# Kernel tuning notes

Measured on AMD Instinct MI355X. Metric: run time of the kernel, lower is better.

The kernel has to match this reference:

```python
import jax, jax.numpy as jnp
import numpy as np

EPS = 1.55e-5  # tf.math.l2_normalize epsilon semantics: x / sqrt(max(sum(x^2), eps))


def _l2norm_tokens(t):
    # normalize over the token axis (-2), matching tf.math.l2_normalize(axis=-2)
    sq = jnp.sum(t * t, axis=-2, keepdims=True)
    return t * jax.lax.rsqrt(jnp.maximum(sq, EPS))


def setup_inputs() -> dict:
    key = jax.random.key(0)
    ks = jax.random.split(key, 4)
    B, H, W, C = 16, 64, 64, 512
    heads = 8
    return {
        "x": jax.random.normal(ks[0], (B, H, W, C), jnp.float32),
        "qkv_w": jax.random.normal(ks[1], (C, 3 * C), jnp.float32) * (C ** -0.5),
        "q_bias": jnp.zeros((C,), jnp.float32),
        "v_bias": jnp.zeros((C,), jnp.float32),
        "scale": jnp.ones((heads, 1, 1), jnp.float32),
        "proj_w": jax.random.normal(ks[2], (C, C), jnp.float32) * (C ** -0.5),
        "proj_b": jnp.zeros((C,), jnp.float32),
    }


def reference(x, qkv_w, q_bias, v_bias, scale, proj_w, proj_b):
    B, H, W, C = x.shape
    heads = scale.shape[0]
    d = C // heads
    N = H * W

    # 1x1 conv QKV (no conv bias) + concatenated [q_bias, 0, v_bias]
    qkv = jnp.einsum("bhwc,cf->bhwf", x, qkv_w)
    qkv = qkv + jnp.concatenate([q_bias, jnp.zeros_like(q_bias), v_bias])
    # [B, N, heads, 3, d] -> [B, heads, N, 3, d]
    qkv = qkv.reshape(B, N, heads, 3, d).transpose(0, 2, 1, 3, 4)
    q, k, v = qkv[..., 0, :], qkv[..., 1, :], qkv[..., 2, :]  # each [B, heads, N, d]

    q = _l2norm_tokens(q)
    k = _l2norm_tokens(k)

    # channel-attention: [B, heads, d, d]
    attn = jnp.einsum("bhnd,bhne->bhde", q * jnp.exp(scale), k)
    attn = jax.nn.softmax(attn, axis=-1)

    # matmul(attn, v^T) -> [B, heads, d, N]; perm [0,3,1,2] -> [B, N, heads, d]
    out = jnp.einsum("bhde,bhne->bhdn", attn, v)
    out = out.transpose(0, 3, 1, 2).reshape(B, H, W, C)

    # output 1x1 conv projection with bias
    return jnp.einsum("bhwc,cf->bhwf", out, proj_w) + proj_b
```

## Files before the change

kernel.cpp:

```cpp
#include <hip/hip_runtime.h>
#include <stdint.h>
#include <stddef.h>

#define BATCH  16
#define HEADS  8
#define NTOK   4096
#define CDIM   512
#define FDIM   1536

typedef short bf16x8 __attribute__((ext_vector_type(8)));
typedef float fx4    __attribute__((ext_vector_type(4)));

__device__ __forceinline__ uint16_t f2bf(float f) {
    uint32_t u = __float_as_uint(f);
    return (uint16_t)((u + 0x7FFFu + ((u >> 16) & 1u)) >> 16);
}
__device__ __forceinline__ float bf2f(uint16_t u) {
    return __uint_as_float(((uint32_t)u) << 16);
}
__device__ __forceinline__ void gload16(const uint16_t* g, uint16_t* l) {
    __builtin_amdgcn_global_load_lds(
        (const __attribute__((address_space(1))) uint32_t*)(g),
        (__attribute__((address_space(3))) uint32_t*)(l), 16, 0, 0);
}
__device__ __forceinline__ int cidx(int row, int col) {
    return row * 128 + (col ^ ((row & 7) << 3));
}

__global__ void transpose_w_kernel(const float* __restrict__ qkv_w,
                                   const float* __restrict__ proj_w,
                                   uint16_t* __restrict__ Wt,
                                   uint16_t* __restrict__ Pt) {
    __shared__ uint16_t tile[32][33];
    int blk = blockIdx.x;
    const float* src; uint16_t* dst; int W, Hh, r0, c0;
    if (blk < 768) {
        int tr = blk / 48, tc = blk % 48;
        src = qkv_w; dst = Wt; W = 1536; Hh = 512; r0 = tr * 32; c0 = tc * 32;
    } else {
        blk -= 768;
        int tr = blk / 16, tc = blk % 16;
        src = proj_w; dst = Pt; W = 512; Hh = 512; r0 = tr * 32; c0 = tc * 32;
    }
    const int tx = threadIdx.x & 31, ty = threadIdx.x >> 5;
    #pragma unroll
    for (int j = 0; j < 4; j++)
        tile[ty + 8 * j][tx] = f2bf(src[(size_t)(r0 + ty + 8 * j) * W + c0 + tx]);
    __syncthreads();
    #pragma unroll
    for (int j = 0; j < 4; j++)
        dst[(size_t)(c0 + ty + 8 * j) * Hh + r0 + tx] = tile[tx][ty + 8 * j];
}

__global__ void prep_kernel(const float* __restrict__ X,
                            uint16_t* __restrict__ Xb,
                            float* __restrict__ Sqk) {
    const int tid = blockIdx.x * blockDim.x + threadIdx.x;
    const int stride = gridDim.x * blockDim.x;
    for (int i = tid; i < (1 << 22); i += stride) {
        const fx4* src = reinterpret_cast<const fx4*>(X + (size_t)i * 8);
        fx4 v0 = src[0], v1 = src[1];
        union { bf16x8 v; uint16_t u[8]; } pk;
        #pragma unroll
        for (int e = 0; e < 4; e++) { pk.u[e] = f2bf(v0[e]); pk.u[4 + e] = f2bf(v1[e]); }
        reinterpret_cast<bf16x8*>(Xb)[i] = pk.v;
    }
    for (int i = tid; i < 16384; i += stride) Sqk[i] = 0.0f;
}

__global__ __launch_bounds__(256) void gemm_qkv_kernel(
        const uint16_t* __restrict__ Xb, const uint16_t* __restrict__ Wt,
        const float* __restrict__ q_bias, const float* __restrict__ v_bias,
        uint16_t* __restrict__ QT, uint16_t* __restrict__ KT,
        uint16_t* __restrict__ VT,
        float* __restrict__ Sq, float* __restrict__ Sk) {
    __shared__ uint16_t ring[4][8192];
    const int bx = blockIdx.x;
    const int swz = (bx & 7) * 768 + (bx >> 3);
    const int tm = swz / 12, tn = swz % 12;
    const int gm = tm * 128, gn = tn * 128;
    const int b = gm >> 12, tok0 = gm & 4095;
    const int t = threadIdx.x, lane = t & 63, w = t >> 6;
    const int wm = w >> 1, wn = w & 1;
    const int l15 = lane & 15, lg = lane >> 4;
    fx4 acc[4][4] = {};
    const int srow = t >> 2;
    const int scol = (((t & 3) ^ (srow & 3)) << 3);
    const uint16_t* gA = Xb + (size_t)(gm + srow) * 512 + scol;
    const uint16_t* gB = Wt + (size_t)(gn + srow) * 512 + scol;
#define STAGE_QKV(kt_) do {                                                   \
        const int s_ = (kt_) & 3; const int k0_ = (kt_) * 32;                 \
        gload16(gA + k0_,                 &ring[s_][t * 8]);                  \
        gload16(gA + (size_t)64*512 + k0_, &ring[s_][t * 8 + 2048]);          \
        gload16(gB + k0_,                 &ring[s_][4096 + t * 8]);           \
        gload16(gB + (size_t)64*512 + k0_, &ring[s_][4096 + t * 8 + 2048]);   \
    } while (0)
    STAGE_QKV(0); STAGE_QKV(1); STAGE_QKV(2);
    #pragma unroll
    for (int kt = 0; kt < 16; ++kt) {
        if (kt < 14)       asm volatile("s_waitcnt vmcnt(8) lgkmcnt(0)" ::: "memory");
        else if (kt == 14) asm volatile("s_waitcnt vmcnt(4) lgkmcnt(0)" ::: "memory");
        else               asm volatile("s_waitcnt vmcnt(0) lgkmcnt(0)" ::: "memory");
        __builtin_amdgcn_s_barrier();
        if (kt < 13) STAGE_QKV(kt + 3);
        const uint16_t* As = &ring[kt & 3][0];
        const uint16_t* Bs = &ring[kt & 3][4096];
        bf16x8 af[4], bfr[4];
        #pragma unroll
        for (int m = 0; m < 4; m++) {
            const int row = wm * 64 + m * 16 + l15;
            af[m] = *reinterpret_cast<const bf16x8*>(&As[row * 32 + ((lg ^ (row & 3)) << 3)]);
        }
        #pragma unroll
        for (int n = 0; n < 4; n++) {
            const int row = wn * 64 + n * 16 + l15;
            bfr[n] = *reinterpret_cast<const bf16x8*>(&Bs[row * 32 + ((lg ^ (row & 3)) << 3)]);
        }
        __builtin_amdgcn_s_setprio(1);
        #pragma unroll
        for (int m = 0; m < 4; m++)
            #pragma unroll
            for (int n = 0; n < 4; n++)
                acc[m][n] = __builtin_amdgcn_mfma_f32_16x16x32_bf16(
                    af[m], bfr[n], acc[m][n], 0, 0, 0);
        __builtin_amdgcn_s_setprio(0);
    }
#undef STAGE_QKV
    __syncthreads();
    uint16_t* sh = &ring[0][0];
    #pragma unroll
    for (int n = 0; n < 4; n++) {
        const int col = gn + wn * 64 + n * 16 + l15;
        const float bias = (col < 512) ? q_bias[col]
                          : ((col < 1024) ? 0.0f : v_bias[col - 1024]);
        #pragma unroll
        for (int m = 0; m < 4; m++)
            #pragma unroll
            for (int r = 0; r < 4; r++) {
                const int lrow = wm * 64 + m * 16 + lg * 4 + r;
                const int lcol = wn * 64 + n * 16 + l15;
                sh[cidx(lrow, lcol)] = f2bf(acc[m][n][r] + bias);
            }
    }
    __syncthreads();
    const int cc = t >> 7, tloc = t & 127;
    const int u = (gn >> 6) + cc;
    const int h = u / 3, which = u % 3;
    const int bh = b * 8 + h;
    if (which < 2) {
        const int d = tloc & 63, oct = tloc >> 6;
        uint16_t* dst = (which == 0 ? QT : KT)
                        + ((size_t)bh * 64 + d) * 4096 + tok0 + oct * 64;
        float ss = 0.f;
        #pragma unroll
        for (int g = 0; g < 8; g++) {
            union { bf16x8 v; uint16_t u16v[8]; } pk;
            #pragma unroll
            for (int s2 = 0; s2 < 8; s2++) {
                uint16_t val = sh[cidx(oct * 64 + g * 8 + s2, cc * 64 + d)];
                pk.u16v[s2] = val;
                float f = bf2f(val);
                ss += f * f;
            }
            *reinterpret_cast<bf16x8*>(dst + g * 8) = pk.v;
        }
        atomicAdd((which == 0 ? Sq : Sk) + bh * 64 + d, ss);
    } else {
        const int tok = tloc;
        uint16_t* dst = VT + (size_t)(gm + tok) * 512 + h * 64;
        #pragma unroll
        for (int bb = 0; bb < 8; bb++) {
            bf16x8 v = *reinterpret_cast<const bf16x8*>(&sh[cidx(tok, cc * 64 + bb * 8)]);
            *reinterpret_cast<bf16x8*>(dst + bb * 8) = v;
        }
    }
}

__global__ __launch_bounds__(256) void attn_qk_kernel(
        const uint16_t* __restrict__ QT, const uint16_t* __restrict__ KT,
        float* __restrict__ Gpart) {
    __shared__ uint16_t Qs[64 * 128];
    __shared__ uint16_t Ks[64 * 128];
    const int blk = blockIdx.x;
    const int bh = blk >> 2, quarter = blk & 3;
    const int t = threadIdx.x, lane = t & 63, w = t >> 6;
    const int l15 = lane & 15, lg = lane >> 4;
    const int wr = w >> 1, wc = w & 1;
    fx4 acc[2][2] = {};
    const uint16_t* qbase = QT + (size_t)bh * 64 * 4096;
    const uint16_t* kbase = KT + (size_t)bh * 64 * 4096;
    for (int it = 0; it < 8; it++) {
        const int tokt = quarter * 1024 + it * 128;
        #pragma unroll
        for (int j = 0; j < 4; j++) {
            const int li = j * 256 + t;
            const int row = li >> 4;
            const int src_off = (((li & 15) ^ (row & 7)) << 3);
            gload16(qbase + (size_t)row * 4096 + tokt + src_off, &Qs[li * 8]);
            gload16(kbase + (size_t)row * 4096 + tokt + src_off, &Ks[li * 8]);
        }
        __syncthreads();
        #pragma unroll
        for (int ks = 0; ks < 4; ks++) {
            const int kof = ks * 32 + lg * 8;
            const int ra0 = wr * 32 + l15,      ra1 = wr * 32 + 16 + l15;
            const int rb0 = wc * 32 + l15,      rb1 = wc * 32 + 16 + l15;
            bf16x8 a0 = *reinterpret_cast<const bf16x8*>(&Qs[ra0 * 128 + (kof ^ ((ra0 & 7) << 3))]);
            bf16x8 a1 = *reinterpret_cast<const bf16x8*>(&Qs[ra1 * 128 + (kof ^ ((ra1 & 7) << 3))]);
            bf16x8 b0 = *reinterpret_cast<const bf16x8*>(&Ks[rb0 * 128 + (kof ^ ((rb0 & 7) << 3))]);
            bf16x8 b1 = *reinterpret_cast<const bf16x8*>(&Ks[rb1 * 128 + (kof ^ ((rb1 & 7) << 3))]);
            acc[0][0] = __builtin_amdgcn_mfma_f32_16x16x32_bf16(a0, b0, acc[0][0], 0, 0, 0);
            acc[0][1] = __builtin_amdgcn_mfma_f32_16x16x32_bf16(a0, b1, acc[0][1], 0, 0, 0);
            acc[1][0] = __builtin_amdgcn_mfma_f32_16x16x32_bf16(a1, b0, acc[1][0], 0, 0, 0);
            acc[1][1] = __builtin_amdgcn_mfma_f32_16x16x32_bf16(a1, b1, acc[1][1], 0, 0, 0);
        }
        __syncthreads();
    }
    float* gp = Gpart + (size_t)quarter * 524288 + (size_t)bh * 4096;
    #pragma unroll
    for (int mi = 0; mi < 2; mi++)
        #pragma unroll
        for (int ni = 0; ni < 2; ni++)
            #pragma unroll
            for (int r = 0; r < 4; r++) {
                const int d = wr * 32 + mi * 16 + lg * 4 + r;
                const int e = wc * 32 + ni * 16 + l15;
                gp[d * 64 + e] = acc[mi][ni][r];
            }
}

__global__ void attn_finalize_kernel(const float* __restrict__ Gpart,
                                     const float* __restrict__ Sq,
                                     const float* __restrict__ Sk,
                                     const float* __restrict__ scale,
                                     uint16_t* __restrict__ attnb) {
    const int bh = blockIdx.x;
    const int h = bh & 7;
    const int t = threadIdx.x;
    const int e = t & 63, w = t >> 6;
    const float es = expf(scale[h]);
    const float rk = rsqrtf(fmaxf(Sk[bh * 64 + e], 1.55e-5f));
    const float* g0 = Gpart + (size_t)bh * 4096;
    for (int d = w; d < 64; d += 4) {
        const float rq = rsqrtf(fmaxf(Sq[bh * 64 + d], 1.55e-5f));
        float g = g0[d * 64 + e] + g0[524288 + d * 64 + e]
                + g0[1048576 + d * 64 + e] + g0[1572864 + d * 64 + e];
        float x = es * g * rq * rk;
        float m = x;
        #pragma unroll
        for (int off = 32; off; off >>= 1) m = fmaxf(m, __shfl_xor(m, off, 64));
        float p = expf(x - m);
        float s = p;
        #pragma unroll
        for (int off = 32; off; off >>= 1) s += __shfl_xor(s, off, 64);
        attnb[(size_t)bh * 4096 + d * 64 + e] = f2bf(p / s);
    }
}

__global__ __launch_bounds__(256) void pv_kernel(
        const uint16_t* __restrict__ VT, const uint16_t* __restrict__ attnb,
        uint16_t* __restrict__ out_t) {
    __shared__ uint16_t Vs[64 * 64];
    __shared__ uint16_t Os[64 * 64];
    const int blk = blockIdx.x;
    const int bh = blk >> 6, chunk = blk & 63;
    const int b = bh >> 3, h = bh & 7;
    const int n0 = chunk * 64;
    const int t = threadIdx.x, lane = t & 63, w = t >> 6;
    const int l15 = lane & 15, lg = lane >> 4;
    #pragma unroll
    for (int j = 0; j < 2; j++) {
        const int li = j * 256 + t;
        const int row = li >> 3;
        const int src_off = (((li & 7) ^ (row & 7)) << 3);
        gload16(VT + (size_t)(b * NTOK + n0 + row) * 512 + h * 64 + src_off, &Vs[li * 8]);
    }
    bf16x8 bfr[4][2];
    const uint16_t* ab = attnb + (size_t)bh * 4096;
    #pragma unroll
    for (int n = 0; n < 4; n++)
        #pragma unroll
        for (int ks = 0; ks < 2; ks++)
            bfr[n][ks] = *reinterpret_cast<const bf16x8*>(ab + (n * 16 + l15) * 64 + ks * 32 + lg * 8);
    __syncthreads();
    fx4 acc[4] = {};
    #pragma unroll
    for (int ks = 0; ks < 2; ks++) {
        const int row = w * 16 + l15;
        const int kof = ks * 32 + lg * 8;
        bf16x8 a = *reinterpret_cast<const bf16x8*>(&Vs[row * 64 + (kof ^ ((row & 7) << 3))]);
        #pragma unroll
        for (int n = 0; n < 4; n++)
            acc[n] = __builtin_amdgcn_mfma_f32_16x16x32_bf16(a, bfr[n][ks], acc[n], 0, 0, 0);
    }
    #pragma unroll
    for (int n = 0; n < 4; n++)
        #pragma unroll
        for (int r = 0; r < 4; r++) {
            const int row = w * 16 + lg * 4 + r;
            const int col = n * 16 + l15;
            Os[row * 64 + (col ^ ((row & 7) << 3))] = f2bf(acc[n][r]);
        }
    __syncthreads();
    {
        const int tr = t >> 2, c0 = (t & 3) * 16;
        uint16_t* orow = out_t + (size_t)(b * NTOK + n0 + tr) * CDIM + h * 64;
        #pragma unroll
        for (int cc2 = 0; cc2 < 2; cc2++) {
            const int c = c0 + cc2 * 8;
            const int chnk = (c >> 3) ^ (tr & 7);
            bf16x8 vv = *reinterpret_cast<const bf16x8*>(&Os[tr * 64 + (chnk << 3)]);
            *reinterpret_cast<bf16x8*>(orow + c) = vv;
        }
    }
}

__global__ __launch_bounds__(256) void gemm_proj_kernel(
        const uint16_t* __restrict__ At, const uint16_t* __restrict__ Pt,
        const float* __restrict__ proj_b, float* __restrict__ outp) {
    __shared__ uint16_t ring[4][8192];
    const int bx = blockIdx.x;
    const int swz = (bx & 7) * 256 + (bx >> 3);
    const int tn = swz & 3, tm = swz >> 2;
    const int gm = tm * 128, gn = tn * 128;
    const int t = threadIdx.x, lane = t & 63, w = t >> 6;
    const int wm = w >> 1, wn = w & 1;
    const int l15 = lane & 15, lg = lane >> 4;
    fx4 acc[4][4] = {};
    const int srow = t >> 2;
    const int scol = (((t & 3) ^ (srow & 3)) << 3);
    const uint16_t* gA = At + (size_t)(gm + srow) * 512 + scol;
    const uint16_t* gB = Pt + (size_t)(gn + srow) * 512 + scol;
#define STAGE_PROJ(kt_) do {                                                  \
        const int s_ = (kt_) & 3; const int k0_ = (kt_) * 32;                 \
        gload16(gA + k0_,                 &ring[s_][t * 8]);                  \
        gload16(gA + (size_t)64*512 + k0_, &ring[s_][t * 8 + 2048]);          \
        gload16(gB + k0_,                 &ring[s_][4096 + t * 8]);           \
        gload16(gB + (size_t)64*512 + k0_, &ring[s_][4096 + t * 8 + 2048]);   \
    } while (0)
    STAGE_PROJ(0); STAGE_PROJ(1); STAGE_PROJ(2);
    #pragma unroll
    for (int kt = 0; kt < 16; ++kt) {
        if (kt < 14)       asm volatile("s_waitcnt vmcnt(8) lgkmcnt(0)" ::: "memory");
        else if (kt == 14) asm volatile("s_waitcnt vmcnt(4) lgkmcnt(0)" ::: "memory");
        else               asm volatile("s_waitcnt vmcnt(0) lgkmcnt(0)" ::: "memory");
        __builtin_amdgcn_s_barrier();
        if (kt < 13) STAGE_PROJ(kt + 3);
        const uint16_t* As = &ring[kt & 3][0];
        const uint16_t* Bs = &ring[kt & 3][4096];
        bf16x8 af[4], bfr[4];
        #pragma unroll
        for (int m = 0; m < 4; m++) {
            const int row = wm * 64 + m * 16 + l15;
            af[m] = *reinterpret_cast<const bf16x8*>(&As[row * 32 + ((lg ^ (row & 3)) << 3)]);
        }
        #pragma unroll
        for (int n = 0; n < 4; n++) {
            const int row = wn * 64 + n * 16 + l15;
            bfr[n] = *reinterpret_cast<const bf16x8*>(&Bs[row * 32 + ((lg ^ (row & 3)) << 3)]);
        }
        __builtin_amdgcn_s_setprio(1);
        #pragma unroll
        for (int m = 0; m < 4; m++)
            #pragma unroll
            for (int n = 0; n < 4; n++)
                acc[m][n] = __builtin_amdgcn_mfma_f32_16x16x32_bf16(
                    af[m], bfr[n], acc[m][n], 0, 0, 0);
        __builtin_amdgcn_s_setprio(0);
    }
#undef STAGE_PROJ
    #pragma unroll
    for (int m = 0; m < 4; m++) {
        #pragma unroll
        for (int n = 0; n < 4; n++) {
            const int col = gn + wn * 64 + n * 16 + l15;
            const float bias = proj_b[col];
            #pragma unroll
            for (int r = 0; r < 4; r++) {
                const int row = gm + wm * 64 + m * 16 + lg * 4 + r;
                outp[(size_t)row * CDIM + col] = acc[m][n][r] + bias;
            }
        }
    }
}

extern "C" void kernel_launch(void* const* d_in, const int* in_sizes, int n_in,
                              void* d_out, int out_size, void* d_ws, size_t ws_size,
                              hipStream_t stream) {
    (void)in_sizes; (void)n_in; (void)out_size; (void)ws_size;
    const float* x      = (const float*)d_in[0];
    const float* qkv_w  = (const float*)d_in[1];
    const float* q_bias = (const float*)d_in[2];
    const float* v_bias = (const float*)d_in[3];
    const float* scale  = (const float*)d_in[4];
    const float* proj_w = (const float*)d_in[5];
    const float* proj_b = (const float*)d_in[6];
    float* out = (float*)d_out;

    char* wsp = (char*)d_ws;
    uint16_t* Wt    = (uint16_t*)(wsp);
    uint16_t* Pt    = (uint16_t*)(wsp + 1572864);
    float*    Sq    = (float*)   (wsp + 2097152);
    float*    Sk    = (float*)   (wsp + 2129920);
    float*    Gpart = (float*)   (wsp + 2162688);
    uint16_t* attnb = (uint16_t*)(wsp + 10551296);
    uint16_t* QT    = (uint16_t*)(wsp + 11599872);
    uint16_t* KT    = (uint16_t*)(wsp + 78708736);
    uint16_t* VT    = (uint16_t*)(wsp + 145817600);
    uint16_t* Xb    = (uint16_t*)(wsp + 212926464);
    uint16_t* out_t = Xb;

    hipLaunchKernelGGL(transpose_w_kernel, dim3(1024), dim3(256), 0, stream,
                       qkv_w, proj_w, Wt, Pt);
    hipLaunchKernelGGL(prep_kernel, dim3(2048), dim3(256), 0, stream,
                       x, Xb, Sq);
    hipLaunchKernelGGL(gemm_qkv_kernel, dim3(6144), dim3(256), 0, stream,
                       Xb, Wt, q_bias, v_bias, QT, KT, VT, Sq, Sk);
    hipLaunchKernelGGL(attn_qk_kernel, dim3(512), dim3(256), 0, stream,
                       QT, KT, Gpart);
    hipLaunchKernelGGL(attn_finalize_kernel, dim3(128), dim3(256), 0, stream,
                       Gpart, Sq, Sk, scale, attnb);
    hipLaunchKernelGGL(pv_kernel, dim3(8192), dim3(256), 0, stream,
                       VT, attnb, out_t);
    hipLaunchKernelGGL(gemm_proj_kernel, dim3(2048), dim3(256), 0, stream,
                       out_t, Pt, proj_b, out);
}
```

Before: 545.5 us.

## Shrink GEMM rings to three stages, store Q/K directly, double-buffer QK loads

The QKV and projection GEMMs drop from a 4-stage to a 3-stage LDS ring (prefetch distance 2). This cuts shared memory per block from 64KB to 48KB so more blocks can be resident. The QKV epilogue now writes Q/K straight from accumulators with 8-byte stores and a shuffle-reduced sum of squares, staging only V through LDS. It also computes the norm from fp32 values rather than rounded bf16. attn_qk gains a double-buffered LDS pipeline so the next token tile loads while the current one computes, at the cost of doubled LDS there.

```diff
diff --git a/kernel.cpp b/kernel.cpp
--- a/kernel.cpp
+++ b/kernel.cpp
@@ -22,9 +22,6 @@
     __builtin_amdgcn_global_load_lds(
         (const __attribute__((address_space(1))) uint32_t*)(g),
         (__attribute__((address_space(3))) uint32_t*)(l), 16, 0, 0);
-}
-__device__ __forceinline__ int cidx(int row, int col) {
-    return row * 128 + (col ^ ((row & 7) << 3));
 }
 
 __global__ void transpose_w_kernel(const float* __restrict__ qkv_w,
@@ -74,7 +71,7 @@
         uint16_t* __restrict__ QT, uint16_t* __restrict__ KT,
         uint16_t* __restrict__ VT,
         float* __restrict__ Sq, float* __restrict__ Sk) {
-    __shared__ uint16_t ring[4][8192];
+    __shared__ uint16_t ring[3][8192];
     const int bx = blockIdx.x;
     const int swz = (bx & 7) * 768 + (bx >> 3);
     const int tm = swz / 12, tn = swz % 12;
@@ -88,23 +85,23 @@
     const int scol = (((t & 3) ^ (srow & 3)) << 3);
     const uint16_t* gA = Xb + (size_t)(gm + srow) * 512 + scol;
     const uint16_t* gB = Wt + (size_t)(gn + srow) * 512 + scol;
-#define STAGE_QKV(kt_) do {                                                   \
-        const int s_ = (kt_) & 3; const int k0_ = (kt_) * 32;                 \
-        gload16(gA + k0_,                 &ring[s_][t * 8]);                  \
-        gload16(gA + (size_t)64*512 + k0_, &ring[s_][t * 8 + 2048]);          \
-        gload16(gB + k0_,                 &ring[s_][4096 + t * 8]);           \
-        gload16(gB + (size_t)64*512 + k0_, &ring[s_][4096 + t * 8 + 2048]);   \
-    } while (0)
-    STAGE_QKV(0); STAGE_QKV(1); STAGE_QKV(2);
+    auto stage = [&](int kt_) {
+        const int s_ = kt_ % 3;
+        const int k0_ = kt_ * 32;
+        gload16(gA + k0_,                    &ring[s_][t * 8]);
+        gload16(gA + (size_t)64 * 512 + k0_, &ring[s_][t * 8 + 2048]);
+        gload16(gB + k0_,                    &ring[s_][4096 + t * 8]);
+        gload16(gB + (size_t)64 * 512 + k0_, &ring[s_][4096 + t * 8 + 2048]);
+    };
+    stage(0); stage(1);
     #pragma unroll
     for (int kt = 0; kt < 16; ++kt) {
-        if (kt < 14)       asm volatile("s_waitcnt vmcnt(8) lgkmcnt(0)" ::: "memory");
-        else if (kt == 14) asm volatile("s_waitcnt vmcnt(4) lgkmcnt(0)" ::: "memory");
-        else               asm volatile("s_waitcnt vmcnt(0) lgkmcnt(0)" ::: "memory");
+        if (kt < 15) asm volatile("s_waitcnt vmcnt(4) lgkmcnt(0)" ::: "memory");
+        else         asm volatile("s_waitcnt vmcnt(0) lgkmcnt(0)" ::: "memory");
         __builtin_amdgcn_s_barrier();
-        if (kt < 13) STAGE_QKV(kt + 3);
-        const uint16_t* As = &ring[kt & 3][0];
-        const uint16_t* Bs = &ring[kt & 3][4096];
+        if (kt < 14) stage(kt + 2);
+        const uint16_t* As = &ring[kt % 3][0];
+        const uint16_t* Bs = &ring[kt % 3][4096];
         bf16x8 af[4], bfr[4];
         #pragma unroll
         for (int m = 0; m < 4; m++) {
@@ -125,53 +122,72 @@
                     af[m], bfr[n], acc[m][n], 0, 0, 0);
         __builtin_amdgcn_s_setprio(0);
     }
-#undef STAGE_QKV
     __syncthreads();
-    uint16_t* sh = &ring[0][0];
+    const int u = (gn >> 6) + wn;
+    const int type = u % 3;
+    const int h = u / 3;
+    const int bh = b * 8 + h;
+    float biasn[4];
     #pragma unroll
     for (int n = 0; n < 4; n++) {
         const int col = gn + wn * 64 + n * 16 + l15;
-        const float bias = (col < 512) ? q_bias[col]
-                          : ((col < 1024) ? 0.0f : v_bias[col - 1024]);
-        #pragma unroll
-        for (int m = 0; m < 4; m++)
-            #pragma unroll
-            for (int r = 0; r < 4; r++) {
-                const int lrow = wm * 64 + m * 16 + lg * 4 + r;
-                const int lcol = wn * 64 + n * 16 + l15;
-                sh[cidx(lrow, lcol)] = f2bf(acc[m][n][r] + bias);
+        biasn[n] = (col < 512) ? q_bias[col]
+                  : ((col < 1024) ? 0.0f : v_bias[col - 1024]);
+    }
+    if (type < 2) {
+        uint16_t* T = (type == 0) ? QT : KT;
+        #pragma unroll
+        for (int n = 0; n < 4; n++) {
+            const int d = n * 16 + l15;
+            uint16_t* dst = T + ((size_t)bh * 64 + d) * 4096 + tok0 + wm * 64 + lg * 4;
+            float ss = 0.f;
+            #pragma unroll
+            for (int m = 0; m < 4; m++) {
+                union { uint16_t u4[4]; uint64_t q; } pk;
+                #pragma unroll
+                for (int r = 0; r < 4; r++) {
+                    const float f = acc[m][n][r] + biasn[n];
+                    pk.u4[r] = f2bf(f);
+                    ss += f * f;
+                }
+                *reinterpret_cast<uint64_t*>(dst + m * 16) = pk.q;
             }
+            ss += __shfl_xor(ss, 16, 64);
+            ss += __shfl_xor(ss, 32, 64);
+            if (lg == 0)
+                atomicAdd((type == 0 ? Sq : Sk) + bh * 64 + d, ss);
+        }
+    } else {
+        uint16_t* vs = &ring[0][0];
+        #pragma unroll
+        for (int n = 0; n < 4; n++) {
+            const int lcol = n * 16 + l15;
+            #pragma unroll
+            for (int m = 0; m < 4; m++)
+                #pragma unroll
+                for (int r = 0; r < 4; r++) {
+                    const int lrow = wm * 64 + m * 16 + lg * 4 + r;
+                    vs[lrow * 64 + (lcol ^ ((lrow & 7) << 3))] =
+                        f2bf(acc[m][n][r] + biasn[n]);
+                }
+        }
     }
     __syncthreads();
-    const int cc = t >> 7, tloc = t & 127;
-    const int u = (gn >> 6) + cc;
-    const int h = u / 3, which = u % 3;
-    const int bh = b * 8 + h;
-    if (which < 2) {
-        const int d = tloc & 63, oct = tloc >> 6;
-        uint16_t* dst = (which == 0 ? QT : KT)
-                        + ((size_t)bh * 64 + d) * 4096 + tok0 + oct * 64;
-        float ss = 0.f;
-        #pragma unroll
-        for (int g = 0; g < 8; g++) {
-            union { bf16x8 v; uint16_t u16v[8]; } pk;
-            #pragma unroll
-            for (int s2 = 0; s2 < 8; s2++) {
-                uint16_t val = sh[cidx(oct * 64 + g * 8 + s2, cc * 64 + d)];
-                pk.u16v[s2] = val;
-                float f = bf2f(val);
-                ss += f * f;
+    {
+        const int u0 = gn >> 6;
+        const int uv = (u0 % 3 == 2) ? u0 : (((u0 + 1) % 3 == 2) ? (u0 + 1) : -1);
+        if (uv >= 0) {
+            const uint16_t* vs = &ring[0][0];
+            const int hv = uv / 3;
+            const int row = t >> 1, c0v = (t & 1) * 32;
+            uint16_t* dst = VT + (size_t)(gm + row) * 512 + hv * 64 + c0v;
+            #pragma unroll
+            for (int cc = 0; cc < 4; cc++) {
+                const int col = c0v + cc * 8;
+                bf16x8 vv = *reinterpret_cast<const bf16x8*>(
+                    &vs[row * 64 + (col ^ ((row & 7) << 3))]);
+                *reinterpret_cast<bf16x8*>(dst + cc * 8) = vv;
             }
-            *reinterpret_cast<bf16x8*>(dst + g * 8) = pk.v;
-        }
-        atomicAdd((which == 0 ? Sq : Sk) + bh * 64 + d, ss);
-    } else {
-        const int tok = tloc;
-        uint16_t* dst = VT + (size_t)(gm + tok) * 512 + h * 64;
-        #pragma unroll
-        for (int bb = 0; bb < 8; bb++) {
-            bf16x8 v = *reinterpret_cast<const bf16x8*>(&sh[cidx(tok, cc * 64 + bb * 8)]);
-            *reinterpret_cast<bf16x8*>(dst + bb * 8) = v;
         }
     }
 }
@@ -179,8 +195,8 @@
 __global__ __launch_bounds__(256) void attn_qk_kernel(
         const uint16_t* __restrict__ QT, const uint16_t* __restrict__ KT,
         float* __restrict__ Gpart) {
-    __shared__ uint16_t Qs[64 * 128];
-    __shared__ uint16_t Ks[64 * 128];
+    __shared__ uint16_t Qs[2][8192];
+    __shared__ uint16_t Ks[2][8192];
     const int blk = blockIdx.x;
     const int bh = blk >> 2, quarter = blk & 3;
     const int t = threadIdx.x, lane = t & 63, w = t >> 6;
@@ -189,32 +205,40 @@
     fx4 acc[2][2] = {};
     const uint16_t* qbase = QT + (size_t)bh * 64 * 4096;
     const uint16_t* kbase = KT + (size_t)bh * 64 * 4096;
-    for (int it = 0; it < 8; it++) {
-        const int tokt = quarter * 1024 + it * 128;
+    auto stage = [&](int it_) {
+        const int tokt = quarter * 1024 + it_ * 128;
+        uint16_t* qd = &Qs[it_ & 1][0];
+        uint16_t* kd = &Ks[it_ & 1][0];
         #pragma unroll
         for (int j = 0; j < 4; j++) {
             const int li = j * 256 + t;
             const int row = li >> 4;
             const int src_off = (((li & 15) ^ (row & 7)) << 3);
-            gload16(qbase + (size_t)row * 4096 + tokt + src_off, &Qs[li * 8]);
-            gload16(kbase + (size_t)row * 4096 + tokt + src_off, &Ks[li * 8]);
-        }
-        __syncthreads();
+            gload16(qbase + (size_t)row * 4096 + tokt + src_off, qd + li * 8);
+            gload16(kbase + (size_t)row * 4096 + tokt + src_off, kd + li * 8);
+        }
+    };
+    stage(0);
+    for (int it = 0; it < 8; it++) {
+        asm volatile("s_waitcnt vmcnt(0) lgkmcnt(0)" ::: "memory");
+        __builtin_amdgcn_s_barrier();
+        if (it < 7) stage(it + 1);
+        const uint16_t* Qb = &Qs[it & 1][0];
+        const uint16_t* Kb = &Ks[it & 1][0];
         #pragma unroll
         for (int ks = 0; ks < 4; ks++) {
             const int kof = ks * 32 + lg * 8;
             const int ra0 = wr * 32 + l15,      ra1 = wr * 32 + 16 + l15;
             const int rb0 = wc * 32 + l15,      rb1 = wc * 32 + 16 + l15;
-            bf16x8 a0 = *reinterpret_cast<const bf16x8*>(&Qs[ra0 * 128 + (kof ^ ((ra0 & 7) << 3))]);
-            bf16x8 a1 = *reinterpret_cast<const bf16x8*>(&Qs[ra1 * 128 + (kof ^ ((ra1 & 7) << 3))]);
-            bf16x8 b0 = *reinterpret_cast<const bf16x8*>(&Ks[rb0 * 128 + (kof ^ ((rb0 & 7) << 3))]);
-            bf16x8 b1 = *reinterpret_cast<const bf16x8*>(&Ks[rb1 * 128 + (kof ^ ((rb1 & 7) << 3))]);
+            bf16x8 a0 = *reinterpret_cast<const bf16x8*>(&Qb[ra0 * 128 + (kof ^ ((ra0 & 7) << 3))]);
+            bf16x8 a1 = *reinterpret_cast<const bf16x8*>(&Qb[ra1 * 128 + (kof ^ ((ra1 & 7) << 3))]);
+            bf16x8 b0 = *reinterpret_cast<const bf16x8*>(&Kb[rb0 * 128 + (kof ^ ((rb0 & 7) << 3))]);
+            bf16x8 b1 = *reinterpret_cast<const bf16x8*>(&Kb[rb1 * 128 + (kof ^ ((rb1 & 7) << 3))]);
             acc[0][0] = __builtin_amdgcn_mfma_f32_16x16x32_bf16(a0, b0, acc[0][0], 0, 0, 0);
             acc[0][1] = __builtin_amdgcn_mfma_f32_16x16x32_bf16(a0, b1, acc[0][1], 0, 0, 0);
             acc[1][0] = __builtin_amdgcn_mfma_f32_16x16x32_bf16(a1, b0, acc[1][0], 0, 0, 0);
             acc[1][1] = __builtin_amdgcn_mfma_f32_16x16x32_bf16(a1, b1, acc[1][1], 0, 0, 0);
         }
-        __syncthreads();
     }
     float* gp = Gpart + (size_t)quarter * 524288 + (size_t)bh * 4096;
     #pragma unroll
@@ -318,7 +342,7 @@
 __global__ __launch_bounds__(256) void gemm_proj_kernel(
         const uint16_t* __restrict__ At, const uint16_t* __restrict__ Pt,
         const float* __restrict__ proj_b, float* __restrict__ outp) {
-    __shared__ uint16_t ring[4][8192];
+    __shared__ uint16_t ring[3][8192];
     const int bx = blockIdx.x;
     const int swz = (bx & 7) * 256 + (bx >> 3);
     const int tn = swz & 3, tm = swz >> 2;
@@ -331,23 +355,23 @@
     const int scol = (((t & 3) ^ (srow & 3)) << 3);
     const uint16_t* gA = At + (size_t)(gm + srow) * 512 + scol;
     const uint16_t* gB = Pt + (size_t)(gn + srow) * 512 + scol;
-#define STAGE_PROJ(kt_) do {                                                  \
-        const int s_ = (kt_) & 3; const int k0_ = (kt_) * 32;                 \
-        gload16(gA + k0_,                 &ring[s_][t * 8]);                  \
-        gload16(gA + (size_t)64*512 + k0_, &ring[s_][t * 8 + 2048]);          \
-        gload16(gB + k0_,                 &ring[s_][4096 + t * 8]);           \
-        gload16(gB + (size_t)64*512 + k0_, &ring[s_][4096 + t * 8 + 2048]);   \
-    } while (0)
-    STAGE_PROJ(0); STAGE_PROJ(1); STAGE_PROJ(2);
+    auto stage = [&](int kt_) {
+        const int s_ = kt_ % 3;
+        const int k0_ = kt_ * 32;
+        gload16(gA + k0_,                    &ring[s_][t * 8]);
+        gload16(gA + (size_t)64 * 512 + k0_, &ring[s_][t * 8 + 2048]);
+        gload16(gB + k0_,                    &ring[s_][4096 + t * 8]);
+        gload16(gB + (size_t)64 * 512 + k0_, &ring[s_][4096 + t * 8 + 2048]);
+    };
+    stage(0); stage(1);
     #pragma unroll
     for (int kt = 0; kt < 16; ++kt) {
-        if (kt < 14)       asm volatile("s_waitcnt vmcnt(8) lgkmcnt(0)" ::: "memory");
-        else if (kt == 14) asm volatile("s_waitcnt vmcnt(4) lgkmcnt(0)" ::: "memory");
-        else               asm volatile("s_waitcnt vmcnt(0) lgkmcnt(0)" ::: "memory");
+        if (kt < 15) asm volatile("s_waitcnt vmcnt(4) lgkmcnt(0)" ::: "memory");
+        else         asm volatile("s_waitcnt vmcnt(0) lgkmcnt(0)" ::: "memory");
         __builtin_amdgcn_s_barrier();
-        if (kt < 13) STAGE_PROJ(kt + 3);
-        const uint16_t* As = &ring[kt & 3][0];
-        const uint16_t* Bs = &ring[kt & 3][4096];
+        if (kt < 14) stage(kt + 2);
+        const uint16_t* As = &ring[kt % 3][0];
+        const uint16_t* Bs = &ring[kt % 3][4096];
         bf16x8 af[4], bfr[4];
         #pragma unroll
         for (int m = 0; m < 4; m++) {
@@ -368,7 +392,6 @@
                     af[m], bfr[n], acc[m][n], 0, 0, 0);
         __builtin_amdgcn_s_setprio(0);
     }
-#undef STAGE_PROJ
     #pragma unroll
     for (int m = 0; m < 4; m++) {
         #pragma unroll
```

New measurement: 531.2 us. 1.03x faster.
